# Kernel optimization log

Measured on AMD Instinct MI355X. Metric: run time of the kernel, lower is better.

The kernel has to match this reference:

```python
import jax, jax.numpy as jnp
import numpy as np

B, N, CIN = 8, 1024, 2048
HID, HC, LV = 1024, 64, 512
NH_SSD, HD, DS = 16, 128, 64
DCONV = 4

def layernorm(x, w, b, eps=1e-5):
    m = x.mean(-1, keepdims=True)
    v = ((x - m) ** 2).mean(-1, keepdims=True)
    return (x - m) * jax.lax.rsqrt(v + eps) * w + b

def rmsnorm(x, w, eps=1e-5):
    return x * jax.lax.rsqrt((x * x).mean(-1, keepdims=True) + eps) * w

def segsum(a):
    # a: (..., T) -> (..., T, T); [i,j] = sum_{j<k<=i} a[k]; -inf above diagonal
    T = a.shape[-1]
    cs = jnp.cumsum(a, -1)
    seg = cs[..., :, None] - cs[..., None, :]
    i = jnp.arange(T)
    return jnp.where(i[:, None] >= i[None, :], seg, -jnp.inf)

def mha(x, Wq, Wk, Wv, Wo, Wo_b, nh=4):
    b, s, h = x.shape
    hd = h // nh
    q = (x @ Wq.T).reshape(b, s, nh, hd).transpose(0, 2, 1, 3)
    k = (x @ Wk.T).reshape(b, s, nh, hd).transpose(0, 2, 1, 3)
    v = (x @ Wv.T).reshape(b, s, nh, hd).transpose(0, 2, 1, 3)
    att = jax.nn.softmax(jnp.einsum('bhqd,bhkd->bhqk', q, k) / jnp.sqrt(jnp.float32(hd)), axis=-1)
    o = jnp.einsum('bhqk,bhkd->bhqd', att, v).transpose(0, 2, 1, 3).reshape(b, s, h)
    return o @ Wo.T + Wo_b

def ssd_minimal(X, A, Bv, Cv, Lc):
    # faithful ssd_minimal_discrete; Bv/Cv have ngroups=1 broadcast to heads (torch einsum broadcasts size-1 labels)
    b, T, h, p = X.shape
    c = T // Lc
    n = Bv.shape[-1]
    X = X.reshape(b, c, Lc, h, p)
    A = A.reshape(b, c, Lc, h).transpose(0, 3, 1, 2)  # b h c l
    Bv = jnp.broadcast_to(Bv.reshape(b, c, Lc, 1, n), (b, c, Lc, h, n))
    Cv = jnp.broadcast_to(Cv.reshape(b, c, Lc, 1, n), (b, c, Lc, h, n))
    cs = jnp.cumsum(A, -1)
    Lmat = jnp.exp(segsum(A))  # b h c l s
    Yd = jnp.einsum('bclhn,bcshn,bhcls,bcshp->bclhp', Cv, Bv, Lmat, X)
    dstates = jnp.exp(cs[..., -1:] - cs)
    st = jnp.einsum('bclhn,bhcl,bclhp->bchpn', Bv, dstates, X)
    st = jnp.concatenate([jnp.zeros_like(st[:, :1]), st], axis=1)
    dchunk = jnp.exp(segsum(jnp.pad(cs[..., -1], ((0, 0), (0, 0), (1, 0)))))
    st = jnp.einsum('bhzc,bchpn->bzhpn', dchunk, st)[:, :-1]
    Yo = jnp.einsum('bclhn,bchpn,bhcl->bclhp', Cv, st, jnp.exp(cs))
    return (Yd + Yo).reshape(b, T, h, p)

def ssd_block(xc, xproj_W, dt_bias, A_log, D):
    b, l, d = xc.shape
    dtBC = xc @ xproj_W.T
    dt = jax.nn.softplus(dtBC[..., :NH_SSD] + dt_bias)
    Bm = dtBC[..., NH_SSD:NH_SSD + DS]
    Cm = dtBC[..., NH_SSD + DS:]
    A = -jnp.exp(A_log)
    X = xc.reshape(b, l, NH_SSD, HD) * dt[..., None]
    Y = ssd_minimal(X, A * dt, Bm, Cm, l)  # single chunk: Lc = seqlen (as in SSD.forward)
    return Y.reshape(b, l, d) + xc * jnp.repeat(D, HD)

@jax.custom_vjp
def round3(y):
    return jnp.round(y)

def _r3_fwd(y):
    return jnp.round(y), y

def _r3_bwd(y, g):
    return (g * (y != 0).astype(g.dtype),)

round3.defvjp(_r3_fwd, _r3_bwd)

def _forward(x, ln0_w, ln0_b, in_W, rms_w, exp_W, conv_W, xproj_W, dt_bias, A_log, D,
             outp_W, outp_b, n1_w, n1_b, aWq, aWk, aWv, aWo, aWo_b,
             h_W, h_b, h_lnw, h_lnb, mask_token, e2d_W, dn_w, dn_b,
             bWq, bWk, bWv, bWo, bWo_b, dout_W, dout_b, mask):
    b = x.shape[0]
    # visible tokens: mask==False; stable argsort keeps original order (== x[~mask].reshape(B,-1,C))
    vis = jnp.argsort(mask.astype(jnp.int32), axis=1)[:, :LV]
    xv = jnp.take_along_axis(x, vis[:, :, None], axis=1)
    xv = layernorm(xv, ln0_w, ln0_b)
    h = xv @ in_W.T
    t = h
    h = rmsnorm(h, rms_w)
    xz = h @ exp_W.T
    xs, z = xz[..., :2 * HID], xz[..., 2 * HID:]
    xc = jax.lax.conv_general_dilated(
        xs.transpose(0, 2, 1), conv_W, (1,), [(DCONV - 1, DCONV - 1)],
        dimension_numbers=('NCH', 'OIH', 'NCH'), feature_group_count=HID)[:, :, :LV].transpose(0, 2, 1)
    y = ssd_block(xc, xproj_W, dt_bias, A_log, D)
    y = y * jax.nn.silu(z)
    y = y @ outp_W.T + outp_b + t
    y = y + mha(layernorm(y, n1_w, n1_b), aWq, aWk, aWv, aWo, aWo_b)
    # hash layer: LN -> hard sigmoid -> straight-through round -> {-1,+1}
    hc = layernorm(y @ h_W.T + h_b, h_lnw, h_lnb)
    hc = 2.0 * round3(jnp.clip((hc + 1.0) / 2.0, 0.0, 1.0)) - 1.0
    # decoder: visible codes + mask tokens
    Lm = N - LV
    dx = jnp.concatenate([hc, jnp.broadcast_to(mask_token, (b, Lm, HC))], axis=1)
    dx = dx @ e2d_W.T
    dx = dx + mha(layernorm(dx, dn_w, dn_b), bWq, bWk, bWv, bWo, bWo_b)
    out = dx @ dout_W.T + dout_b
    return out[:, -Lm:]

def setup_inputs():
    key = jax.random.key(0)
    ks = jax.random.split(key, 20)
    r = lambda i, shape, s=0.02: jax.random.normal(ks[i], shape, dtype=jnp.float32) * s
    x = jax.random.normal(ks[0], (B, N, CIN), dtype=jnp.float32)
    mask = jnp.concatenate([jnp.zeros((B, LV), bool), jnp.ones((B, N - LV), bool)], axis=1)
    A = jax.random.uniform(ks[1], (NH_SSD,), minval=1.0, maxval=16.0)
    return dict(
        x=x,
        ln0_w=jnp.ones(CIN), ln0_b=jnp.zeros(CIN),
        in_W=r(2, (HID, CIN)),
        rms_w=jnp.ones(HID),
        exp_W=r(3, (4 * HID, HID)),
        conv_W=r(4, (2 * HID, 2, DCONV), 0.1),
        xproj_W=r(5, (NH_SSD + 2 * DS, 2 * HID)),
        dt_bias=jnp.zeros(NH_SSD), A_log=jnp.log(A), D=jnp.ones(NH_SSD),
        outp_W=r(6, (HID, 2 * HID)), outp_b=jnp.zeros(HID),
        n1_w=jnp.ones(HID), n1_b=jnp.zeros(HID),
        aWq=r(7, (HID, HID)), aWk=r(8, (HID, HID)), aWv=r(9, (HID, HID)),
        aWo=r(10, (HID, HID)), aWo_b=jnp.zeros(HID),
        h_W=r(11, (HC, HID)), h_b=jnp.zeros(HC),
        h_lnw=jnp.ones(HC), h_lnb=jnp.zeros(HC),
        mask_token=jnp.zeros((1, 1, HC)),
        e2d_W=r(12, (HID, HC)),
        dn_w=jnp.ones(HID), dn_b=jnp.zeros(HID),
        bWq=r(13, (HID, HID)), bWk=r(14, (HID, HID)), bWv=r(15, (HID, HID)),
        bWo=r(16, (HID, HID)), bWo_b=jnp.zeros(HID),
        dout_W=r(17, (CIN, HID)), dout_b=jnp.zeros(CIN),
        mask=mask)

def reference(x, ln0_w, ln0_b, in_W, rms_w, exp_W, conv_W, xproj_W, dt_bias, A_log, D,
              outp_W, outp_b, n1_w, n1_b, aWq, aWk, aWv, aWo, aWo_b,
              h_W, h_b, h_lnw, h_lnb, mask_token, e2d_W, dn_w, dn_b,
              bWq, bWk, bWv, bWo, bWo_b, dout_W, dout_b, mask):
    return _forward(x, ln0_w, ln0_b, in_W, rms_w, exp_W, conv_W, xproj_W, dt_bias, A_log, D,
                    outp_W, outp_b, n1_w, n1_b, aWq, aWk, aWv, aWo, aWo_b,
                    h_W, h_b, h_lnw, h_lnb, mask_token, e2d_W, dn_w, dn_b,
                    bWq, bWk, bWv, bWo, bWo_b, dout_W, dout_b, mask)
```

## Files before the change

### kernel.cpp

```cpp
#include <hip/hip_runtime.h>


typedef short bf16x8 __attribute__((ext_vector_type(8)));
typedef float f32x4 __attribute__((ext_vector_type(4)));

__device__ __forceinline__ unsigned short bf16_rne(float f) {
    unsigned u = __float_as_uint(f);
    unsigned r = u + 0x7FFFu + ((u >> 16) & 1u);
    return (unsigned short)(r >> 16);
}
__device__ __forceinline__ float bf16_tof(unsigned short h) {
    return __uint_as_float(((unsigned)h) << 16);
}
__device__ __forceinline__ void store_pair(unsigned short* dst, long long row,
                                           int width, int c, float v) {
    unsigned short hi = bf16_rne(v);
    unsigned short lo = bf16_rne(v - bf16_tof(hi));
    long long base = row * (2LL * width);
    dst[base + c] = hi;
    dst[base + width + c] = lo;
}
__device__ __forceinline__ void async_ld16(const unsigned short* g, unsigned short* l) {
    __builtin_amdgcn_global_load_lds(
        (const __attribute__((address_space(1))) unsigned int*)g,
        (__attribute__((address_space(3))) unsigned int*)l, 16, 0, 0);
}

__device__ __forceinline__ float block_sum256(float v) {
    #pragma unroll
    for (int o = 32; o > 0; o >>= 1) v += __shfl_xor(v, o, 64);
    __shared__ float sm[4];
    int w = threadIdx.x >> 6;
    __syncthreads();
    if ((threadIdx.x & 63) == 0) sm[w] = v;
    __syncthreads();
    return sm[0] + sm[1] + sm[2] + sm[3];
}
__device__ __forceinline__ float block_max256(float v) {
    #pragma unroll
    for (int o = 32; o > 0; o >>= 1) v = fmaxf(v, __shfl_xor(v, o, 64));
    __shared__ float smx[4];
    int w = threadIdx.x >> 6;
    __syncthreads();
    if ((threadIdx.x & 63) == 0) smx[w] = v;
    __syncthreads();
    return fmaxf(fmaxf(smx[0], smx[1]), fmaxf(smx[2], smx[3]));
}

template<int NPASS, int OUT, bool DIRECT>
__global__ __launch_bounds__(256, 2) void gemm_bf16_k(
    int M, int N, int K,
    const unsigned short* __restrict__ A2, int lda2, int aLo, long long sAb, long long sAh,
    const unsigned short* __restrict__ B2, int ldb2, int bLo, long long sBb, long long sBh,
    void* __restrict__ Cv, int ldc, int cLo, long long sCb, long long sCh,
    const float* __restrict__ bias, const float* __restrict__ res, int ldr,
    float alpha, int nh)
{
    constexpr int ST   = DIRECT ? 32 : 40;
    constexpr int NARR = (NPASS == 3) ? 4 : 2;
    constexpr int NB   = DIRECT ? 2 : 1;
    constexpr int O_AH = 0;
    constexpr int O_BH = 128 * ST;
    constexpr int O_AL = 2 * 128 * ST;
    constexpr int O_BL = 3 * 128 * ST;
    constexpr int BUFSZ = 128 * ST * NARR;
    __shared__ unsigned short SM[NB * BUFSZ];

    const int z  = blockIdx.z;
    const int bb = z / nh, hh = z - bb * nh;
    A2 += bb * sAb + hh * sAh;
    B2 += bb * sBb + hh * sBh;

    const int t    = threadIdx.x;
    const int m0   = blockIdx.y * 128;
    const int n0   = blockIdx.x * 128;
    const int lane = t & 63, wave = t >> 6;
    const int wm   = (wave >> 1) * 64, wn = (wave & 1) * 64;
    const int lr   = lane & 15, quad = lane >> 4;

    f32x4 acc[4][4];
    #pragma unroll
    for (int i = 0; i < 4; ++i)
        #pragma unroll
        for (int j = 0; j < 4; ++j) acc[i][j] = (f32x4){0.f, 0.f, 0.f, 0.f};

    if constexpr (DIRECT) {
        const int drow  = lane >> 2;
        const int dcswz = (((lane & 3) ^ ((lane >> 2) & 3) ^ ((lane >> 4) & 3)) << 3);
        const int rsw   = ((quad ^ ((lr & 3) ^ (lr >> 2))) << 3);

        auto stage = [&](int k0, int buf) {
            unsigned short* bp = &SM[buf * BUFSZ];
            #pragma unroll
            for (int j = 0; j < 2; ++j) {
                int rr = wave * 32 + j * 16;
                int gr = rr + drow;
                const unsigned short* gA = A2 + (long long)(m0 + gr) * lda2 + k0 + dcswz;
                async_ld16(gA, &bp[O_AH + rr * 32]);
                if (NPASS == 3) async_ld16(gA + aLo, &bp[O_AL + rr * 32]);
                const unsigned short* gB = B2 + (long long)(n0 + gr) * ldb2 + k0 + dcswz;
                async_ld16(gB, &bp[O_BH + rr * 32]);
                if (NPASS == 3) async_ld16(gB + bLo, &bp[O_BL + rr * 32]);
            }
        };

        const int nt = K >> 5;
        stage(0, 0);
        int cur = 0;
        for (int it = 0; it < nt; ++it) {
            asm volatile("s_waitcnt vmcnt(0)" ::: "memory");
            __builtin_amdgcn_s_barrier();
            if (it + 1 < nt) stage((it + 1) << 5, cur ^ 1);

            const unsigned short* bp = &SM[cur * BUFSZ];
            bf16x8 ah[4], bh[4], al[4], bl[4];
            #pragma unroll
            for (int i = 0; i < 4; ++i) {
                int ra = O_AH + (wm + i * 16 + lr) * 32 + rsw;
                int rb = O_BH + (wn + i * 16 + lr) * 32 + rsw;
                ah[i] = *(const bf16x8*)&bp[ra];
                bh[i] = *(const bf16x8*)&bp[rb];
                if (NPASS == 3) {
                    al[i] = *(const bf16x8*)&bp[ra + (O_AL - O_AH)];
                    bl[i] = *(const bf16x8*)&bp[rb + (O_BL - O_BH)];
                }
            }
            #pragma unroll
            for (int mi = 0; mi < 4; ++mi)
                #pragma unroll
                for (int ni = 0; ni < 4; ++ni) {
                    acc[mi][ni] = __builtin_amdgcn_mfma_f32_16x16x32_bf16(
                        ah[mi], bh[ni], acc[mi][ni], 0, 0, 0);
                    if (NPASS == 3) {
                        acc[mi][ni] = __builtin_amdgcn_mfma_f32_16x16x32_bf16(
                            al[mi], bh[ni], acc[mi][ni], 0, 0, 0);
                        acc[mi][ni] = __builtin_amdgcn_mfma_f32_16x16x32_bf16(
                            ah[mi], bl[ni], acc[mi][ni], 0, 0, 0);
                    }
                }
            cur ^= 1;
        }
    } else {
        const int srow = t >> 2;
        const int scol = (t & 3) * 8;

        for (int k0 = 0; k0 < K; k0 += 32) {
            __syncthreads();
            #pragma unroll
            for (int half = 0; half < 2; ++half) {
                int r = srow + half * 64;
                const unsigned short* pA = A2 + (long long)(m0 + r) * lda2 + k0 + scol;
                *(uint4*)&SM[O_AH + r * ST + scol] = *(const uint4*)pA;
                if (NPASS == 3)
                    *(uint4*)&SM[O_AL + r * ST + scol] = *(const uint4*)(pA + aLo);
                int rb = n0 + r;
                uint4 vh = {0u, 0u, 0u, 0u}, vl = {0u, 0u, 0u, 0u};
                if (rb < N) {
                    const unsigned short* pB = B2 + (long long)rb * ldb2 + k0 + scol;
// ... 33 lines not shown
        }
    }

    if (OUT == 0) {
        float* C = (float*)Cv + bb * sCb + hh * sCh;
        #pragma unroll
        for (int mi = 0; mi < 4; ++mi)
            #pragma unroll
            for (int ni = 0; ni < 4; ++ni) {
                int col = n0 + wn + ni * 16 + lr;
                if (col >= N) continue;
                float bv = bias ? bias[col] : 0.f;
                #pragma unroll
                for (int r = 0; r < 4; ++r) {
                    int row = m0 + wm + mi * 16 + quad * 4 + r;
                    float v = alpha * acc[mi][ni][r] + bv;
                    if (res) v += res[(long long)row * ldr + col];
                    C[(long long)row * ldc + col] = v;
                }
            }
    } else if (OUT == 1) {
        unsigned short* C = (unsigned short*)Cv + bb * sCb + hh * sCh;
        #pragma unroll
        for (int mi = 0; mi < 4; ++mi)
            #pragma unroll
            for (int ni = 0; ni < 4; ++ni) {
                int col = n0 + wn + ni * 16 + lr;
                if (col >= N) continue;
                float bv = bias ? bias[col] : 0.f;
                #pragma unroll
                for (int r = 0; r < 4; ++r) {
                    int row = m0 + wm + mi * 16 + quad * 4 + r;
                    float v = alpha * acc[mi][ni][r] + bv;
                    if (res) v += res[(long long)row * ldr + col];
                    unsigned short hi = bf16_rne(v);
                    unsigned short lo = bf16_rne(v - bf16_tof(hi));
                    long long p = (long long)row * ldc + col;
                    C[p] = hi;
                    C[p + cLo] = lo;
                }
            }
    } else {
        unsigned short* C = (unsigned short*)Cv;
        #pragma unroll
        for (int mi = 0; mi < 4; ++mi)
            #pragma unroll
            for (int ni = 0; ni < 4; ++ni) {
                int col = n0 + wn + ni * 16 + lr;
                if (col >= N) continue;
                int row0 = m0 + wm + mi * 16 + quad * 4;
                int b = row0 >> 9, seq0 = row0 & 511;
                ushort4 h4, l4;
                unsigned short* hp = (unsigned short*)&h4;
                unsigned short* lp = (unsigned short*)&l4;
                #pragma unroll
                for (int r = 0; r < 4; ++r) {
                    float v = acc[mi][ni][r];
                    unsigned short hi = bf16_rne(v);
                    hp[r] = hi;
                    lp[r] = bf16_rne(v - bf16_tof(hi));
                }
                long long p = b * sCb + (long long)col * ldc + seq0;
                *(ushort4*)&C[p] = h4;
                *(ushort4*)&C[p + cLo] = l4;
            }
    }
}

template<int NPASS, int TR>
__global__ __launch_bounds__(256, 2) void gemm_bf16_skd_k(
    int N, int KC,
    const unsigned short* __restrict__ A2, int lda2, int aLo,
    const unsigned short* __restrict__ B2, int ldb2, int bLo,
    float* __restrict__ P, long long sCk)
{
    constexpr int NARR = (NPASS == 3) ? 4 : 2;
    constexpr int O_AH = 0;
    constexpr int O_BH = 128 * 32;
    constexpr int O_AL = 2 * 128 * 32;
    constexpr int O_BL = 3 * 128 * 32;
    constexpr int BUFSZ = 128 * 32 * NARR;
    __shared__ unsigned short SM[2 * BUFSZ];

    const int t    = threadIdx.x;
    const int m0   = blockIdx.y * 128;
    const int n0   = blockIdx.x * 128;
    const int kbeg = blockIdx.z * KC;
    const int lane = t & 63, wave = t >> 6;
    const int wm   = (wave >> 1) * 64, wn = (wave & 1) * 64;
    const int lr   = lane & 15, quad = lane >> 4;

    f32x4 acc[4][4];
    #pragma unroll
    for (int i = 0; i < 4; ++i)
        #pragma unroll
        for (int j = 0; j < 4; ++j) acc[i][j] = (f32x4){0.f, 0.f, 0.f, 0.f};

    const int drow  = lane >> 2;
    const int dcswz = (((lane & 3) ^ ((lane >> 2) & 3) ^ ((lane >> 4) & 3)) << 3);
    const int rsw   = ((quad ^ ((lr & 3) ^ (lr >> 2))) << 3);

    auto stage = [&](int k0, int buf) {
        unsigned short* bp = &SM[buf * BUFSZ];
        #pragma unroll
        for (int j = 0; j < 2; ++j) {
            int rr = wave * 32 + j * 16;
            int gr = rr + drow;
            const unsigned short* gA = A2 + (long long)(m0 + gr) * lda2 + k0 + dcswz;
            async_ld16(gA, &bp[O_AH + rr * 32]);
            if (NPASS == 3) async_ld16(gA + aLo, &bp[O_AL + rr * 32]);
            const unsigned short* gB = B2 + (long long)(n0 + gr) * ldb2 + k0 + dcswz;
            async_ld16(gB, &bp[O_BH + rr * 32]);
            if (NPASS == 3) async_ld16(gB + bLo, &bp[O_BL + rr * 32]);
        }
    };

    const int nt = KC >> 5;
    stage(kbeg, 0);
    int cur = 0;
    for (int it = 0; it < nt; ++it) {
        asm volatile("s_waitcnt vmcnt(0)" ::: "memory");
        __builtin_amdgcn_s_barrier();
        if (it + 1 < nt) stage(kbeg + ((it + 1) << 5), cur ^ 1);

        const unsigned short* bp = &SM[cur * BUFSZ];
        bf16x8 ah[4], bh[4], al[4], bl[4];
        #pragma unroll
        for (int i = 0; i < 4; ++i) {
            int ra = O_AH + (wm + i * 16 + lr) * 32 + rsw;
            int rb = O_BH + (wn + i * 16 + lr) * 32 + rsw;
            ah[i] = *(const bf16x8*)&bp[ra];
            bh[i] = *(const bf16x8*)&bp[rb];
            if (NPASS == 3) {
                al[i] = *(const bf16x8*)&bp[ra + (O_AL - O_AH)];
                bl[i] = *(const bf16x8*)&bp[rb + (O_BL - O_BH)];
            }
        }
        #pragma unroll
        for (int mi = 0; mi < 4; ++mi)
            #pragma unroll
            for (int ni = 0; ni < 4; ++ni) {
                acc[mi][ni] = __builtin_amdgcn_mfma_f32_16x16x32_bf16(
                    ah[mi], bh[ni], acc[mi][ni], 0, 0, 0);
                if (NPASS == 3) {
                    acc[mi][ni] = __builtin_amdgcn_mfma_f32_16x16x32_bf16(
                        al[mi], bh[ni], acc[mi][ni], 0, 0, 0);
                    acc[mi][ni] = __builtin_amdgcn_mfma_f32_16x16x32_bf16(
                        ah[mi], bl[ni], acc[mi][ni], 0, 0, 0);
                }
            }
        cur ^= 1;
    }

    float* Pc = P + (long long)blockIdx.z * sCk;
    if (TR == 0) {
        #pragma unroll
        for (int mi = 0; mi < 4; ++mi)
            #pragma unroll
            for (int ni = 0; ni < 4; ++ni) {
                int col = n0 + wn + ni * 16 + lr;
                #pragma unroll
                for (int r = 0; r < 4; ++r) {
                    int row = m0 + wm + mi * 16 + quad * 4 + r;
                    Pc[(long long)row * N + col] = acc[mi][ni][r];
                }
            }
    } else {
        #pragma unroll
        for (int mi = 0; mi < 4; ++mi)
            #pragma unroll
            for (int ni = 0; ni < 4; ++ni) {
                int col = n0 + wn + ni * 16 + lr;
                int row0 = m0 + wm + mi * 16 + quad * 4;
                int b = row0 >> 9, seq0 = row0 & 511;
                *(float4*)&Pc[(long long)b * ((long long)N * 512)
                              + (long long)col * 512 + seq0] =
                    *(float4*)&acc[mi][ni];
            }
    }
}

template<int NPASS>
__global__ __launch_bounds__(256, 2) void gemm_bf16_sk_k(
    int N, int KC,
    const unsigned short* __restrict__ A2, int lda2, int aLo,
    const unsigned short* __restrict__ B2, int ldb2, int bLo,
    float* __restrict__ C, long long sCk)
{
    constexpr int ST = 40;
    __shared__ unsigned short Ah[128 * ST];
    __shared__ unsigned short Bh[128 * ST];
    __shared__ unsigned short Al[128 * ST];
    __shared__ unsigned short Bl[128 * ST];

    const int t    = threadIdx.x;
    const int m0   = blockIdx.y * 128;
    const int n0   = blockIdx.x * 128;
    const int kbeg = blockIdx.z * KC;
    const int lane = t & 63, wave = t >> 6;
    const int wm   = (wave >> 1) * 64, wn = (wave & 1) * 64;
    const int lr   = lane & 15, quad = lane >> 4;

    f32x4 acc[4][4];
    #pragma unroll
    for (int i = 0; i < 4; ++i)
        #pragma unroll
        for (int j = 0; j < 4; ++j) acc[i][j] = (f32x4){0.f, 0.f, 0.f, 0.f};

    const int srow = t >> 2;
    const int scol = (t & 3) * 8;

    for (int k0 = kbeg; k0 < kbeg + KC; k0 += 32) {
        __syncthreads();
        #pragma unroll
        for (int half = 0; half < 2; ++half) {
            int r = srow + half * 64;
            const unsigned short* pA = A2 + (long long)(m0 + r) * lda2 + k0 + scol;
            *(uint4*)&Ah[r * ST + scol] = *(const uint4*)pA;
            if (NPASS == 3)
                *(uint4*)&Al[r * ST + scol] = *(const uint4*)(pA + aLo);
            int rb = n0 + r;
            uint4 vh = {0u, 0u, 0u, 0u}, vl = {0u, 0u, 0u, 0u};
            if (rb < N) {
                const unsigned short* pB = B2 + (long long)rb * ldb2 + k0 + scol;
                vh = *(const uint4*)pB;
                if (NPASS == 3) vl = *(const uint4*)(pB + bLo);
            }
            *(uint4*)&Bh[r * ST + scol] = vh;
            if (NPASS == 3) *(uint4*)&Bl[r * ST + scol] = vl;
        }
        __syncthreads();

        bf16x8 ah[4], bh[4], al[4], bl[4];
        #pragma unroll
        for (int i = 0; i < 4; ++i) {
            int ra = (wm + i * 16 + lr) * ST + quad * 8;
            int rb = (wn + i * 16 + lr) * ST + quad * 8;
            ah[i] = *(const bf16x8*)&Ah[ra];
            bh[i] = *(const bf16x8*)&Bh[rb];
            if (NPASS == 3) {
                al[i] = *(const bf16x8*)&Al[ra];
                bl[i] = *(const bf16x8*)&Bl[rb];
            }
        }
        #pragma unroll
        for (int mi = 0; mi < 4; ++mi)
            #pragma unroll
            for (int ni = 0; ni < 4; ++ni) {
                acc[mi][ni] = __builtin_amdgcn_mfma_f32_16x16x32_bf16(
                    ah[mi], bh[ni], acc[mi][ni], 0, 0, 0);
                if (NPASS == 3) {
                    acc[mi][ni] = __builtin_amdgcn_mfma_f32_16x16x32_bf16(
                        al[mi], bh[ni], acc[mi][ni], 0, 0, 0);
                    acc[mi][ni] = __builtin_amdgcn_mfma_f32_16x16x32_bf16(
                        ah[mi], bl[ni], acc[mi][ni], 0, 0, 0);
                }
            }
    }

    float* Cc = C + (long long)blockIdx.z * sCk;
    #pragma unroll
    for (int mi = 0; mi < 4; ++mi)
        #pragma unroll
        for (int ni = 0; ni < 4; ++ni) {
            int col = n0 + wn + ni * 16 + lr;
            if (col >= N) continue;
            #pragma unroll
            for (int r = 0; r < 4; ++r) {
                int row = m0 + wm + mi * 16 + quad * 4 + r;
                Cc[(long long)row * N + col] = acc[mi][ni][r];
            }
        }
}

__global__ __launch_bounds__(256) void skredN_k(
    const float* __restrict__ P, long long sCk, int nchunk,
    const float* __restrict__ bias, const float* __restrict__ res, int ncol,
    float* __restrict__ outp, long long n)
{
    long long idx = (long long)blockIdx.x * 256 + threadIdx.x;
// ... 218 lines not shown

    for (int k0 = 0; k0 < K; k0 += 32) {
        __syncthreads();
        #pragma unroll
        for (int i = 0; i < 4; ++i) {
            int row = m0 + ra + i * 32;
            float4 v = *(const float4*)(A + (long long)row * lda + (k0 + ka));
            As[ka + 0][ra + i * 32] = v.x;
            As[ka + 1][ra + i * 32] = v.y;
            As[ka + 2][ra + i * 32] = v.z;
            As[ka + 3][ra + i * 32] = v.w;
            int rowb = n0 + ra + i * 32;
            float4 w = *(const float4*)(B + (long long)rowb * ldb + (k0 + ka));
            Bs[ka + 0][ra + i * 32] = w.x;
            Bs[ka + 1][ra + i * 32] = w.y;
            Bs[ka + 2][ra + i * 32] = w.z;
            Bs[ka + 3][ra + i * 32] = w.w;
        }
        __syncthreads();
        #pragma unroll
        for (int kk = 0; kk < 32; ++kk) {
            float a[8], bm[8];
            *(float4*)&a[0]  = *(const float4*)&As[kk][ty * 4];
            *(float4*)&a[4]  = *(const float4*)&As[kk][64 + ty * 4];
            *(float4*)&bm[0] = *(const float4*)&Bs[kk][tx * 4];
            *(float4*)&bm[4] = *(const float4*)&Bs[kk][64 + tx * 4];
            #pragma unroll
            for (int ri = 0; ri < 2; ++ri)
                #pragma unroll
                for (int ci = 0; ci < 2; ++ci)
                    #pragma unroll
                    for (int i = 0; i < 4; ++i)
                        #pragma unroll
                        for (int j = 0; j < 4; ++j)
                            acc[ri * 2 + ci][i * 4 + j] =
                                fmaf(a[ri * 4 + i], bm[ci * 4 + j], acc[ri * 2 + ci][i * 4 + j]);
        }
    }
    #pragma unroll
    for (int ri = 0; ri < 2; ++ri)
        #pragma unroll
        for (int ci = 0; ci < 2; ++ci) {
            int colb = n0 + ci * 64 + tx * 4;
            #pragma unroll
            for (int i = 0; i < 4; ++i) {
                int row = m0 + ri * 64 + ty * 4 + i;
                *(float4*)(C + (long long)row * ldc + colb) =
                    *(float4*)&acc[ri * 2 + ci][i * 4];
            }
        }
}

__global__ __launch_bounds__(256) void pairify_k(
    const float* __restrict__ src, unsigned short* __restrict__ dst,
    int k_log2, long long n)
{
    long long idx = (long long)blockIdx.x * 256 + threadIdx.x;
    if (idx >= n) return;
    long long r = idx >> k_log2;
    int c = (int)(idx & ((1 << k_log2) - 1));
    store_pair(dst, r, 1 << k_log2, c, src[idx]);
}

__global__ __launch_bounds__(256) void layernorm_k(
    const float* __restrict__ in, float* __restrict__ out,
    const float* __restrict__ w, const float* __restrict__ b,
    int width, int rows_per_b, long long in_bstride)
{
    long long r = blockIdx.x;
    const float* x = in + (r / rows_per_b) * in_bstride + (r % rows_per_b) * (long long)width;
    int t = threadIdx.x;
    float s = 0.f;
    for (int c = t; c < width; c += 256) s += x[c];
    s = block_sum256(s);
    float m = s / (float)width;
    float vs = 0.f;
    for (int c = t; c < width; c += 256) { float d = x[c] - m; vs += d * d; }
    vs = block_sum256(vs);
    float rs = 1.f / sqrtf(vs / (float)width + 1e-5f);
    float* o = out + r * (long long)width;
    for (int c = t; c < width; c += 256) o[c] = (x[c] - m) * rs * w[c] + b[c];
}

__global__ __launch_bounds__(256) void layernorm_pair_k(
    const float* __restrict__ in, unsigned short* __restrict__ out2,
    const float* __restrict__ w, const float* __restrict__ b,
    int width, int rows_per_b, long long in_bstride)
{
    long long r = blockIdx.x;
    const float* x = in + (r / rows_per_b) * in_bstride + (r % rows_per_b) * (long long)width;
    int t = threadIdx.x;
    float s = 0.f;
    for (int c = t; c < width; c += 256) s += x[c];
    s = block_sum256(s);
    float m = s / (float)width;
    float vs = 0.f;
    for (int c = t; c < width; c += 256) { float d = x[c] - m; vs += d * d; }
    vs = block_sum256(vs);
    float rs = 1.f / sqrtf(vs / (float)width + 1e-5f);
    for (int c = t; c < width; c += 256)
        store_pair(out2, r, width, c, (x[c] - m) * rs * w[c] + b[c]);
}

__global__ __launch_bounds__(256) void rmsnorm_pair_k(
    const float* __restrict__ in, unsigned short* __restrict__ out2,
    const float* __restrict__ w, int width)
{
    long long r = blockIdx.x;
    const float* x = in + r * (long long)width;
    int t = threadIdx.x;
    float s = 0.f;
    for (int c = t; c < width; c += 256) { float v = x[c]; s += v * v; }
    s = block_sum256(s);
    float rs = 1.f / sqrtf(s / (float)width + 1e-5f);
    for (int c = t; c < width; c += 256)
        store_pair(out2, r, width, c, x[c] * rs * w[c]);
}

__global__ __launch_bounds__(256) void softmax_pair_k(float* __restrict__ S,
                                                      unsigned short* __restrict__ P2)
{
    long long r = blockIdx.x;
    float* x = S + r * 512;
    unsigned short* p = P2 + r * 1024;
    int t = threadIdx.x;
    float v0 = x[t], v1 = x[t + 256];
    float mx = block_max256(fmaxf(v0, v1));
    v0 = expf(v0 - mx); v1 = expf(v1 - mx);
    float sum = block_sum256(v0 + v1);
    float inv = 1.f / sum;
    v0 *= inv; v1 *= inv;
    __syncthreads();
    unsigned short h0 = bf16_rne(v0);
    p[t] = h0;       p[512 + t] = bf16_rne(v0 - bf16_tof(h0));
    unsigned short h1 = bf16_rne(v1);
    p[t + 256] = h1; p[512 + t + 256] = bf16_rne(v1 - bf16_tof(h1));
}

__global__ __launch_bounds__(256) void conv_k(
    const float* __restrict__ XS, const float* __restrict__ W,
    unsigned short* __restrict__ XC2, unsigned short* __restrict__ XCT2)
{
    __shared__ float tile[64][65];
    const int o0  = blockIdx.x * 64;
    const int tt0 = blockIdx.y * 64;
    const int b   = blockIdx.z;
    const int t   = threadIdx.x;

    const int o  = o0 + (t & 63);
    const int g2 = (o >> 1) << 1;
    const float* Wo = W + o * 8;
    float w0 = Wo[0], w1 = Wo[1], w2 = Wo[2], w3 = Wo[3];
    float w4 = Wo[4], w5 = Wo[5], w6 = Wo[6], w7 = Wo[7];
    #pragma unroll
    for (int i = 0; i < 16; ++i) {
        int sl = (t >> 6) + 4 * i;
        int tt = tt0 + sl;
        const float* xb = XS + ((long long)(b * 512 + tt)) * 2048 + g2;
        float acc = w3 * xb[0] + w7 * xb[1];
        if (tt >= 1) acc += w2 * xb[-2048] + w6 * xb[-2047];
        if (tt >= 2) acc += w1 * xb[-4096] + w5 * xb[-4095];
        if (tt >= 3) acc += w0 * xb[-6144] + w4 * xb[-6143];
        tile[sl][t & 63] = acc;
    }
    __syncthreads();
    #pragma unroll
    for (int i = 0; i < 16; ++i) {
        int idx = t + 256 * i;
        int sl = idx >> 6, ol = idx & 63;
        float v = tile[sl][ol];
        unsigned short hi = bf16_rne(v);
        unsigned short lo = bf16_rne(v - bf16_tof(hi));
        long long row = (long long)(b * 512 + tt0 + sl);
        XC2[row * 4096 + o0 + ol] = hi;
        XC2[row * 4096 + 2048 + o0 + ol] = lo;
    }
    #pragma unroll
    for (int i = 0; i < 16; ++i) {
        int idx = t + 256 * i;
        int cl = idx >> 6, s = idx & 63;
        float v = tile[s][cl];
        unsigned short hi = bf16_rne(v);
        unsigned short lo = bf16_rne(v - bf16_tof(hi));
        long long tb = (long long)b * 2097152 + (long long)(o0 + cl) * 1024 + tt0 + s;
        XCT2[tb] = hi;
        XCT2[tb + 512] = lo;
    }
}

__global__ __launch_bounds__(256) void dt_k(
    const float* __restrict__ dtBC, const float* __restrict__ dt_bias, float* __restrict__ DT)
{
    int idx = blockIdx.x * 256 + threadIdx.x;
    int r = idx >> 4, h = idx & 15;
    float xv = dtBC[r * 144 + h] + dt_bias[h];
    DT[idx] = (xv > 20.f) ? xv : log1pf(expf(xv));
}

__global__ __launch_bounds__(64) void cuma_k(
// ... 152 lines not shown
}

__global__ __launch_bounds__(256) void bcast_k(
    const float* __restrict__ outm, float* __restrict__ out)
{
    int idx = blockIdx.x * 256 + threadIdx.x;
    int c4 = idx & 511;
    int b = idx >> 18;
    ((float4*)out)[idx] = ((const float4*)outm)[b * 512 + c4];
}

static inline void pairify(hipStream_t s, const float* src, unsigned short* dst,
                           int k_log2, long long n)
{
    pairify_k<<<(int)((n + 255) / 256), 256, 0, s>>>(src, dst, k_log2, n);
}

extern "C" void kernel_launch(void* const* d_in, const int* in_sizes, int n_in,
                              void* d_out, int out_size, void* d_ws, size_t ws_size,
                              hipStream_t stream)
{
    const float* x       = (const float*)d_in[0];
    const float* ln0_w   = (const float*)d_in[1];
    const float* ln0_b   = (const float*)d_in[2];
    const float* in_W    = (const float*)d_in[3];
    const float* rms_w   = (const float*)d_in[4];
    const float* exp_W   = (const float*)d_in[5];
    const float* conv_W  = (const float*)d_in[6];
    const float* xproj_W = (const float*)d_in[7];
    const float* dt_bias = (const float*)d_in[8];
    const float* A_log   = (const float*)d_in[9];
    const float* Dv      = (const float*)d_in[10];
    const float* outp_W  = (const float*)d_in[11];
    const float* outp_b  = (const float*)d_in[12];
    const float* n1_w    = (const float*)d_in[13];
    const float* n1_b    = (const float*)d_in[14];
    const float* aWq     = (const float*)d_in[15];
    const float* aWk     = (const float*)d_in[16];
    const float* aWv     = (const float*)d_in[17];
    const float* aWo     = (const float*)d_in[18];
    const float* aWo_b   = (const float*)d_in[19];
    const float* h_W     = (const float*)d_in[20];
    const float* h_b     = (const float*)d_in[21];
    const float* h_lnw   = (const float*)d_in[22];
    const float* h_lnb   = (const float*)d_in[23];
    const float* mtok    = (const float*)d_in[24];
    const float* e2d_W   = (const float*)d_in[25];
    const float* dn_w    = (const float*)d_in[26];
    const float* dn_b    = (const float*)d_in[27];
    const float* bWq     = (const float*)d_in[28];
    const float* bWk     = (const float*)d_in[29];
    const float* bWv     = (const float*)d_in[30];
    const float* bWo     = (const float*)d_in[31];
    const float* bWo_b   = (const float*)d_in[32];
    const float* dout_W  = (const float*)d_in[33];
    const float* dout_b  = (const float*)d_in[34];

    float* ws  = (float*)d_ws;
    float* out = (float*)d_out;

    float* S1 = ws;
    float* S2 = ws + 8388608;
    float* S3 = ws + 16777216;
    float* S4 = ws + 25165824;
    float* S5 = ws + 33554432;
    float* S6 = ws + 37748736;
    float* S7 = ws + 41943040;
    float* S8 = ws + 46137344;
    float* S9 = ws + 50331648;
    float* SP = ws + 54525952;

    unsigned short* XV2     = (unsigned short*)S1;
    unsigned short* exp_W2  = (unsigned short*)S1;
    unsigned short* XCT2    = (unsigned short*)S1;
    float*          POUTP   = S1;
    float*          SA      = S1;
    unsigned short* P2      = (unsigned short*)S1;
    float*          KVm     = S1;
    unsigned short* in_W2   = (unsigned short*)S2;
    float*          XS      = S2;
    unsigned short* YS2     = (unsigned short*)S2;
    float*          PX      = S2;
    unsigned short* QKA2    = (unsigned short*)S2;
    float*          PB      = S2;
    unsigned short* XC2     = (unsigned short*)S3;
    float*          PIN     = S3;
    unsigned short* outp_W2 = (unsigned short*)S3;
    float*          PATT    = S3;
    float*          PH      = S3;
    float*          DXV     = S3;
    unsigned short* LNDXV2  = (unsigned short*)(S3 + 4194304);
    float*          Z       = S4;
    unsigned short* aWq2    = (unsigned short*)S4;
    unsigned short* aWk2    = (unsigned short*)S4 + 2097152;
    unsigned short* aWv2    = (unsigned short*)S4 + 4194304;
    unsigned short* aWo2    = (unsigned short*)S4 + 6291456;
    unsigned short* bWk2    = (unsigned short*)S4 + 8388608;
    unsigned short* bWv2    = (unsigned short*)S4 + 10485760;
    float*          T       = S5;
    unsigned short* Y22     = (unsigned short*)S5;
    unsigned short* HR2     = (unsigned short*)S6;
    float*          Y1      = S6;
    unsigned short* LNY2    = (unsigned short*)S7;
    unsigned short* OA2     = (unsigned short*)S7;
    unsigned short* VT2     = (unsigned short*)S9;

    float* dtBC = SP;
    float* DT   = SP + 589824;
    float* CUMA = SP + 655360;
    float* G    = SP + 720896;
    unsigned short* xprojW2 = (unsigned short*)(SP + 2818048);
    unsigned short* hW2     = (unsigned short*)(SP + 3112960);
    unsigned short* e2dW2   = (unsigned short*)(SP + 3178496);
    float* G1   = SP + 720896;
    unsigned short* HCQ2 = (unsigned short*)(SP + 983040);
    float* dxm  = SP + 1245184;
    float* lnm  = SP + 1246208;
    float* qm   = SP + 1247232;
    float* km   = SP + 1248256;
    float* vm   = SP + 1249280;
    float* OBm  = SP + 1250304;
    float* ydm  = SP + 1258496;
    float* outm = SP + 1266688;

    const long long LL0 = 0;
    const long long P4M = 4194304;
    #define G3D(OUTM, GX, GY, GZ, ...) \
        gemm_bf16_k<3, OUTM, true><<<dim3(GX, GY, GZ), 256, 0, stream>>>(__VA_ARGS__)
    #define G1D(OUTM, GX, GY, GZ, ...) \
        gemm_bf16_k<1, OUTM, true><<<dim3(GX, GY, GZ), 256, 0, stream>>>(__VA_ARGS__)

    pairify(stream, in_W,    in_W2,   11, 1024LL * 2048);
    pairify(stream, xproj_W, xprojW2, 11, 144LL * 2048);
    pairify(stream, h_W,     hW2,     10, 64LL * 1024);
    pairify(stream, e2d_W,   e2dW2,    6, 1024LL * 64);

    layernorm_pair_k<<<4096, 256, 0, stream>>>(x, XV2, ln0_w, ln0_b, 2048, 512,
                                               (long long)1024 * 2048);
    gemm_bf16_skd_k<3, 0><<<dim3(8, 32, 2), 256, 0, stream>>>(
        1024, 1024, XV2, 4096, 2048, in_W2, 4096, 2048, PIN, P4M);
    skredN_k<<<16384, 256, 0, stream>>>(PIN, P4M, 2, nullptr, nullptr, 1024,
                                        T, P4M);
    pairify(stream, exp_W, exp_W2, 10, 4096LL * 1024);
    rmsnorm_pair_k<<<4096, 256, 0, stream>>>(T, HR2, rms_w, 1024);
    G3D(0, 16, 32, 1, 4096, 2048, 1024, HR2, 2048, 1024, LL0, LL0,
        exp_W2, 2048, 1024, LL0, LL0, XS, 2048, 0, LL0, LL0,
        nullptr, nullptr, 0, 1.f, 1);
    G3D(0, 16, 32, 1, 4096, 2048, 1024, HR2, 2048, 1024, LL0, LL0,
        exp_W2 + 2048LL * 2048, 2048, 1024, LL0, LL0, Z, 2048, 0, LL0, LL0,
        nullptr, nullptr, 0, 1.f, 1);
    conv_k<<<dim3(32, 8, 8), 256, 0, stream>>>(XS, conv_W, XC2, XCT2);
    gemm_bf16_sk_k<3><<<dim3(2, 32, 8), 256, 0, stream>>>(
        144, 256, XC2, 4096, 2048, xprojW2, 4096, 2048, PX, 589824LL);
    skredN_k<<<2304, 256, 0, stream>>>(PX, 589824LL, 8, nullptr, nullptr, 144,
                                       dtBC, 589824LL);
    dt_k<<<256, 256, 0, stream>>>(dtBC, dt_bias, DT);
    cuma_k<<<dim3(16, 8), 64, 0, stream>>>(DT, A_log, CUMA);
    gemm_f32_k<<<dim3(4, 4, 8), 256, 0, stream>>>(
        512, 512, 64, dtBC + 80, 144, (long long)512 * 144,
        dtBC + 16, 144, (long long)512 * 144, G, 512, (long long)512 * 512);
    ssd_mfma_k<<<dim3(4, 16, 8), 256, 0, stream>>>(G, CUMA, DT, XCT2, Z, Dv, YS2);

    pairify(stream, outp_W, outp_W2, 11, 1024LL * 2048);
    pairify(stream, aWq, aWq2, 10, 1024LL * 1024);
    pairify(stream, aWk, aWk2, 10, 1024LL * 1024);
    pairify(stream, aWv, aWv2, 10, 1024LL * 1024);
    pairify(stream, aWo, aWo2, 10, 1024LL * 1024);
    pairify(stream, bWk, bWk2, 10, 1024LL * 1024);
    pairify(stream, bWv, bWv2, 10, 1024LL * 1024);

    gemm_bf16_skd_k<3, 0><<<dim3(8, 32, 2), 256, 0, stream>>>(
        1024, 1024, YS2, 4096, 2048, outp_W2, 4096, 2048, POUTP, P4M);
    skredN_k<<<16384, 256, 0, stream>>>(POUTP, P4M, 2, outp_b, T, 1024,
                                        Y1, P4M);

    layernorm_pair_k<<<4096, 256, 0, stream>>>(Y1, LNY2, n1_w, n1_b, 1024, 4096, LL0);
    G3D(1, 16, 32, 1, 4096, 2048, 1024, LNY2, 2048, 1024, LL0, LL0,
        aWq2, 2048, 1024, LL0, LL0, QKA2, 4096, 2048, LL0, LL0,
        nullptr, nullptr, 0, 1.f, 1);
    gemm_bf16_skd_k<3, 1><<<dim3(8, 32, 2), 256, 0, stream>>>(
        1024, 512, LNY2, 2048, 1024, aWv2, 2048, 1024, PATT, P4M);
    skredT_k<<<16384, 256, 0, stream>>>(PATT, P4M, 2, VT2, P4M);
    G3D(0, 4, 4, 32, 512, 512, 256,
        QKA2, 4096, 2048, (long long)512 * 4096, 256,
        QKA2 + 1024, 4096, 2048, (long long)512 * 4096, 256,
        SA, 512, 0, (long long)4 * 512 * 512, (long long)512 * 512,
        nullptr, nullptr, 0, 1.f / 16.f, 4);
    softmax_pair_k<<<16384, 256, 0, stream>>>(SA, P2);
    G3D(1, 2, 4, 32, 512, 256, 512,
        P2, 1024, 512, (long long)4 * 512 * 1024, (long long)512 * 1024,
        VT2, 1024, 512, (long long)1024 * 1024, (long long)256 * 1024,
        OA2, 2048, 1024, (long long)512 * 2048, 256,
        nullptr, nullptr, 0, 1.f, 4);
    gemm_bf16_skd_k<3, 0><<<dim3(8, 32, 2), 256, 0, stream>>>(
        1024, 512, OA2, 2048, 1024, aWo2, 2048, 1024, PATT, P4M);
    skredP_k<<<16384, 256, 0, stream>>>(PATT, P4M, 2, aWo_b, Y1, Y22, P4M);

    gemm_bf16_sk_k<3><<<dim3(1, 32, 8), 256, 0, stream>>>(
        64, 128, Y22, 2048, 1024, hW2, 2048, 1024, PH, 262144LL);
    skredN_k<<<1024, 256, 0, stream>>>(PH, 262144LL, 8, h_b, nullptr, 64,
                                       G1, 262144LL);
    hc_quant_k<<<4096, 64, 0, stream>>>(G1, h_lnw, h_lnb, HCQ2);

    G3D(0, 8, 32, 1, 4096, 1024, 64, HCQ2, 128, 64, LL0, LL0,
        e2dW2, 128, 64, LL0, LL0, DXV, 1024, 0, LL0, LL0,
        nullptr, nullptr, 0, 1.f, 1);
    dxm_k<<<4, 256, 0, stream>>>(mtok, e2d_W, dxm);
    layernorm_k<<<1, 256, 0, stream>>>(dxm, lnm, dn_w, dn_b, 1024, 1, LL0);
    layernorm_pair_k<<<4096, 256, 0, stream>>>(DXV, LNDXV2, dn_w, dn_b, 1024, 4096, LL0);
    projm_k<<<12, 256, 0, stream>>>(lnm, bWq, bWk, bWv, qm, km, vm);
    G1D(0, 16, 32, 1, 4096, 2048, 1024, LNDXV2, 2048, 1024, LL0, LL0,
        bWk2, 2048, 1024, LL0, LL0, KVm, 2048, 0, LL0, LL0,
        nullptr, nullptr, 0, 1.f, 1);
    dec_attn_k<<<dim3(4, 8), 256, 0, stream>>>(KVm, qm, km, vm, OBm);
    ydm_k<<<32, 256, 0, stream>>>(OBm, bWo, bWo_b, dxm, ydm);
    outm_k<<<64, 256, 0, stream>>>(ydm, dout_W, dout_b, outm);
    bcast_k<<<8192, 256, 0, stream>>>(outm, out);
    #undef G3D
    #undef G1D
}
```

Baseline: 1.096 ms.

## Remap GEMM tiles across XCDs, vectorize norm kernels, batch expansion GEMMs

Adds an XCD-aware block index remap to the three bf16 GEMM kernels so that neighbouring output tiles land on the same chiplet and share L2. Replaces the layernorm and rmsnorm pair kernels with templated versions that read each row once with float4 loads and keep it in registers, instead of reading it from global memory three times. Merges the two expansion-projection GEMMs (XS and Z) into one batched launch using grid z. The remap only applies when the grid size is divisible by eight, and the new norm kernels assume the row width is a multiple of 1024.

```diff
diff --git a/kernel.cpp b/kernel.cpp
--- a/kernel.cpp
+++ b/kernel.cpp
@@ -24,6 +24,16 @@
     __builtin_amdgcn_global_load_lds(
         (const __attribute__((address_space(1))) unsigned int*)g,
         (__attribute__((address_space(3))) unsigned int*)l, 16, 0, 0);
+}
+
+__device__ __forceinline__ void xcd_remap(int& bx, int& by) {
+    const int Gx = gridDim.x;
+    const int nwg = Gx * gridDim.y;
+    if ((nwg & 7) != 0) return;
+    int lin = bx + Gx * by;
+    int logical = (lin & 7) * (nwg >> 3) + (lin >> 3);
+    bx = logical % Gx;
+    by = logical / Gx;
 }
 
 __device__ __forceinline__ float block_sum256(float v) {
@@ -71,9 +81,11 @@
     A2 += bb * sAb + hh * sAh;
     B2 += bb * sBb + hh * sBh;
 
+    int bx = blockIdx.x, by = blockIdx.y;
+    xcd_remap(bx, by);
     const int t    = threadIdx.x;
-    const int m0   = blockIdx.y * 128;
-    const int n0   = blockIdx.x * 128;
+    const int m0   = by * 128;
+    const int n0   = bx * 128;
     const int lane = t & 63, wave = t >> 6;
     const int wm   = (wave >> 1) * 64, wn = (wave & 1) * 64;
     const int lr   = lane & 15, quad = lane >> 4;
@@ -273,9 +285,11 @@
     constexpr int BUFSZ = 128 * 32 * NARR;
     __shared__ unsigned short SM[2 * BUFSZ];
 
+    int bx = blockIdx.x, by = blockIdx.y;
+    xcd_remap(bx, by);
     const int t    = threadIdx.x;
-    const int m0   = blockIdx.y * 128;
-    const int n0   = blockIdx.x * 128;
+    const int m0   = by * 128;
+    const int n0   = bx * 128;
     const int kbeg = blockIdx.z * KC;
     const int lane = t & 63, wave = t >> 6;
     const int wm   = (wave >> 1) * 64, wn = (wave & 1) * 64;
@@ -384,9 +398,11 @@
     __shared__ unsigned short Al[128 * ST];
     __shared__ unsigned short Bl[128 * ST];
 
+    int bx = blockIdx.x, by = blockIdx.y;
+    xcd_remap(bx, by);
     const int t    = threadIdx.x;
-    const int m0   = blockIdx.y * 128;
-    const int n0   = blockIdx.x * 128;
+    const int m0   = by * 128;
+    const int n0   = bx * 128;
     const int kbeg = blockIdx.z * KC;
     const int lane = t & 63, wave = t >> 6;
     const int wm   = (wave >> 1) * 64, wn = (wave & 1) * 64;
@@ -771,39 +787,69 @@
     for (int c = t; c < width; c += 256) o[c] = (x[c] - m) * rs * w[c] + b[c];
 }
 
-__global__ __launch_bounds__(256) void layernorm_pair_k(
+template<int NE>
+__global__ __launch_bounds__(256) void layernorm_pair_v_k(
     const float* __restrict__ in, unsigned short* __restrict__ out2,
     const float* __restrict__ w, const float* __restrict__ b,
-    int width, int rows_per_b, long long in_bstride)
-{
+    int rows_per_b, long long in_bstride)
+{
+    const int width = NE * 256;
     long long r = blockIdx.x;
-    const float* x = in + (r / rows_per_b) * in_bstride + (r % rows_per_b) * (long long)width;
-    int t = threadIdx.x;
+    const float* x = in + (r / rows_per_b) * in_bstride
+                   + (r % rows_per_b) * (long long)width;
+    const int t = threadIdx.x;
+    float v[NE];
     float s = 0.f;
-    for (int c = t; c < width; c += 256) s += x[c];
+    #pragma unroll
+    for (int j = 0; j < NE / 4; ++j) {
+        float4 f = *(const float4*)(x + j * 1024 + t * 4);
+        v[j * 4 + 0] = f.x; v[j * 4 + 1] = f.y;
+        v[j * 4 + 2] = f.z; v[j * 4 + 3] = f.w;
+        s += f.x + f.y + f.z + f.w;
+    }
     s = block_sum256(s);
     float m = s / (float)width;
     float vs = 0.f;
-    for (int c = t; c < width; c += 256) { float d = x[c] - m; vs += d * d; }
+    #pragma unroll
+    for (int e = 0; e < NE; ++e) { float d = v[e] - m; vs += d * d; }
     vs = block_sum256(vs);
     float rs = 1.f / sqrtf(vs / (float)width + 1e-5f);
-    for (int c = t; c < width; c += 256)
-        store_pair(out2, r, width, c, (x[c] - m) * rs * w[c] + b[c]);
-}
-
-__global__ __launch_bounds__(256) void rmsnorm_pair_k(
+    #pragma unroll
+    for (int j = 0; j < NE / 4; ++j)
+        #pragma unroll
+        for (int e = 0; e < 4; ++e) {
+            int c = j * 1024 + t * 4 + e;
+            store_pair(out2, r, width, c, (v[j * 4 + e] - m) * rs * w[c] + b[c]);
+        }
+}
+
+template<int NE>
+__global__ __launch_bounds__(256) void rmsnorm_pair_v_k(
     const float* __restrict__ in, unsigned short* __restrict__ out2,
-    const float* __restrict__ w, int width)
-{
+    const float* __restrict__ w)
+{
+    const int width = NE * 256;
     long long r = blockIdx.x;
     const float* x = in + r * (long long)width;
-    int t = threadIdx.x;
+    const int t = threadIdx.x;
+    float v[NE];
     float s = 0.f;
-    for (int c = t; c < width; c += 256) { float v = x[c]; s += v * v; }
+    #pragma unroll
+    for (int j = 0; j < NE / 4; ++j) {
+        float4 f = *(const float4*)(x + j * 1024 + t * 4);
+        v[j * 4 + 0] = f.x; v[j * 4 + 1] = f.y;
+        v[j * 4 + 2] = f.z; v[j * 4 + 3] = f.w;
+        s += f.x * f.x + f.y * f.y + f.z * f.z + f.w * f.w;
+    }
     s = block_sum256(s);
     float rs = 1.f / sqrtf(s / (float)width + 1e-5f);
-    for (int c = t; c < width; c += 256)
-        store_pair(out2, r, width, c, x[c] * rs * w[c]);
+    #pragma unroll
+    for (int j = 0; j < NE / 4; ++j)
+        #pragma unroll
+        for (int e = 0; e < 4; ++e) {
+            int c = j * 1024 + t * 4 + e;
+            store_pair(out2, r, width, c, v[j * 4 + e] * rs * w[c]);
+        }
 }
 
 __global__ __launch_bounds__(256) void softmax_pair_k(float* __restrict__ S,
@@ -1122,7 +1168,6 @@
     unsigned short* YS2     = (unsigned short*)S2;
     float*          PX      = S2;
     unsigned short* QKA2    = (unsigned short*)S2;
-    float*          PB      = S2;
     unsigned short* XC2     = (unsigned short*)S3;
     float*          PIN     = S3;
     unsigned short* outp_W2 = (unsigned short*)S3;
@@ -1175,19 +1220,17 @@
     pairify(stream, h_W,     hW2,     10, 64LL * 1024);
     pairify(stream, e2d_W,   e2dW2,    6, 1024LL * 64);
 
-    layernorm_pair_k<<<4096, 256, 0, stream>>>(x, XV2, ln0_w, ln0_b, 2048, 512,
-                                               (long long)1024 * 2048);
+    layernorm_pair_v_k<8><<<4096, 256, 0, stream>>>(x, XV2, ln0_w, ln0_b, 512,
+                                                    (long long)1024 * 2048);
     gemm_bf16_skd_k<3, 0><<<dim3(8, 32, 2), 256, 0, stream>>>(
         1024, 1024, XV2, 4096, 2048, in_W2, 4096, 2048, PIN, P4M);
     skredN_k<<<16384, 256, 0, stream>>>(PIN, P4M, 2, nullptr, nullptr, 1024,
                                         T, P4M);
     pairify(stream, exp_W, exp_W2, 10, 4096LL * 1024);
-    rmsnorm_pair_k<<<4096, 256, 0, stream>>>(T, HR2, rms_w, 1024);
-    G3D(0, 16, 32, 1, 4096, 2048, 1024, HR2, 2048, 1024, LL0, LL0,
-        exp_W2, 2048, 1024, LL0, LL0, XS, 2048, 0, LL0, LL0,
-        nullptr, nullptr, 0, 1.f, 1);
-    G3D(0, 16, 32, 1, 4096, 2048, 1024, HR2, 2048, 1024, LL0, LL0,
-        exp_W2 + 2048LL * 2048, 2048, 1024, LL0, LL0, Z, 2048, 0, LL0, LL0,
+    rmsnorm_pair_v_k<4><<<4096, 256, 0, stream>>>(T, HR2, rms_w);
+    G3D(0, 16, 32, 2, 4096, 2048, 1024, HR2, 2048, 1024, LL0, LL0,
+        exp_W2, 2048, 1024, (long long)2048 * 2048, LL0,
+        XS, 2048, 0, 16777216LL, LL0,
         nullptr, nullptr, 0, 1.f, 1);
     conv_k<<<dim3(32, 8, 8), 256, 0, stream>>>(XS, conv_W, XC2, XCT2);
     gemm_bf16_sk_k<3><<<dim3(2, 32, 8), 256, 0, stream>>>(
@@ -1214,7 +1257,8 @@
     skredN_k<<<16384, 256, 0, stream>>>(POUTP, P4M, 2, outp_b, T, 1024,
                                         Y1, P4M);
 
-    layernorm_pair_k<<<4096, 256, 0, stream>>>(Y1, LNY2, n1_w, n1_b, 1024, 4096, LL0);
+    layernorm_pair_v_k<4><<<4096, 256, 0, stream>>>(Y1, LNY2, n1_w, n1_b,
+                                                    4096, LL0);
     G3D(1, 16, 32, 1, 4096, 2048, 1024, LNY2, 2048, 1024, LL0, LL0,
         aWq2, 2048, 1024, LL0, LL0, QKA2, 4096, 2048, LL0, LL0,
         nullptr, nullptr, 0, 1.f, 1);
@@ -1247,7 +1291,8 @@
         nullptr, nullptr, 0, 1.f, 1);
     dxm_k<<<4, 256, 0, stream>>>(mtok, e2d_W, dxm);
     layernorm_k<<<1, 256, 0, stream>>>(dxm, lnm, dn_w, dn_b, 1024, 1, LL0);
-    layernorm_pair_k<<<4096, 256, 0, stream>>>(DXV, LNDXV2, dn_w, dn_b, 1024, 4096, LL0);
+    layernorm_pair_v_k<4><<<4096, 256, 0, stream>>>(DXV, LNDXV2, dn_w, dn_b,
+                                                    4096, LL0);
     projm_k<<<12, 256, 0, stream>>>(lnm, bWq, bWk, bWv, qm, km, vm);
     G1D(0, 16, 32, 1, 4096, 2048, 1024, LNDXV2, 2048, 1024, LL0, LL0,
         bWk2, 2048, 1024, LL0, LL0, KVm, 2048, 0, LL0, LL0,
```

Result: faster. 1.059 ms (-3.4%).
